# Optimization experiments

Measured on AMD Instinct MI355X. Metric: run time of the kernel, lower is better.

Reference implementation:

```python
import jax, jax.numpy as jnp
import numpy as np

V, D, B, S = 32000, 1024, 4, 2048
EPS = 1e-12  # matches torch F.normalize eps


def setup_inputs() -> dict:
    key = jax.random.key(0)
    k1, k2, k3 = jax.random.split(key, 3)
    init_embed = jax.random.normal(k1, (V, D), dtype=jnp.float32)
    scale = np.sqrt(D).astype(np.float32)  # default scale = sqrt(embed_dim)
    norm = jnp.maximum(jnp.linalg.norm(init_embed, axis=-1, keepdims=True), EPS)
    in_weight = scale * (init_embed / norm)            # [V, D]
    out_weight = init_embed.T                          # [D, V]
    inputs = jax.random.randint(k2, (B, S), 0, V)      # token ids
    embeds = jax.random.normal(k3, (B, S, D), dtype=jnp.float32)
    return {"inputs": inputs, "embeds": embeds, "in_weight": in_weight, "out_weight": out_weight}


def reference(inputs, embeds, in_weight, out_weight):
    # embed(): one_hot @ in_weight is mathematically an index gather
    embedded = jnp.take(in_weight, inputs, axis=0)          # [B, S, D]
    # unembed(): dense matmul against transposed embedding table
    logits = jnp.einsum('bsd,dv->bsv', embeds, out_weight)  # [B, S, V]
    return embedded, logits
```

## Files before the change

### kernel.cpp

```cpp
#include <hip/hip_runtime.h>
#include <hip/hip_bf16.h>
#include <stdint.h>

#define V_SZ 32000
#define D_SZ 1024
#define M_SZ 8192

typedef __attribute__((ext_vector_type(8))) short bf16x8;
typedef __attribute__((ext_vector_type(4))) float f32x4;
typedef __attribute__((ext_vector_type(16))) float f32x16;

static __device__ __forceinline__ unsigned short f32_to_bf16_rne(float f) {
    union { float f; uint32_t u; } v; v.f = f;
    uint32_t u = v.u;
    uint32_t lsb = (u >> 16) & 1;
    u += 0x7fffu + lsb;
    return (unsigned short)(u >> 16);
}

__global__ void gather_rows(const int* __restrict__ ids,
                            const float* __restrict__ table,
                            float* __restrict__ out) {
    int row = blockIdx.x;
    int id  = ids[row];
    const f32x4* src = (const f32x4*)(table + (size_t)id * D_SZ);
    f32x4*       dst = (f32x4*)(out + (size_t)row * D_SZ);
    __builtin_nontemporal_store(src[threadIdx.x], &dst[threadIdx.x]);
}

__global__ void cast_f32_bf16(const float* __restrict__ in,
                              unsigned short* __restrict__ out, int n8) {
    int i = blockIdx.x * blockDim.x + threadIdx.x;
    int stride = gridDim.x * blockDim.x;
    for (; i < n8; i += stride) {
        const float4* p = (const float4*)(in + (size_t)i * 8);
        float4 a = p[0], b = p[1];
        union { unsigned short s[8]; uint4 v; } r;
        r.s[0] = f32_to_bf16_rne(a.x); r.s[1] = f32_to_bf16_rne(a.y);
        r.s[2] = f32_to_bf16_rne(a.z); r.s[3] = f32_to_bf16_rne(a.w);
        r.s[4] = f32_to_bf16_rne(b.x); r.s[5] = f32_to_bf16_rne(b.y);
        r.s[6] = f32_to_bf16_rne(b.z); r.s[7] = f32_to_bf16_rne(b.w);
        ((uint4*)out)[i] = r.v;
    }
}

__global__ void transpose_cast(const float* __restrict__ w,
                               unsigned short* __restrict__ bt) {
    __shared__ unsigned short tile[32][34];
    int n0 = blockIdx.x * 32;
    int k0 = blockIdx.y * 32;
    int r = threadIdx.x >> 5;
    int c = threadIdx.x & 31;
#pragma unroll
    for (int rr = 0; rr < 32; rr += 8) {
        float v = w[(size_t)(k0 + r + rr) * V_SZ + (n0 + c)];
        tile[c][r + rr] = f32_to_bf16_rne(v);
    }
    __syncthreads();
    int nl = threadIdx.x >> 3;
    int ks = threadIdx.x & 7;
    union { unsigned short s[4]; uint2 v; } r2;
#pragma unroll
    for (int j = 0; j < 4; ++j) r2.s[j] = tile[nl][ks * 4 + j];
    ((uint2*)(bt + (size_t)(n0 + nl) * D_SZ + k0))[ks] = r2.v;
}

#define BM 256
#define BN 256
#define BK 64
#define NSTEP (D_SZ / BK)

static __device__ __forceinline__ void gload_lds16(const unsigned short* g, void* lds) {
    __builtin_amdgcn_global_load_lds(
        (const __attribute__((address_space(1))) void*)g,
        (__attribute__((address_space(3))) void*)lds,
        16, 0, 0);
}

__global__ __launch_bounds__(512, 2)
void gemm_persist(const unsigned short* __restrict__ A,
                  const unsigned short* __restrict__ Bt,
                  float* __restrict__ C) {
    __shared__ __align__(16) char lds[131072];

    const int tid  = threadIdx.x;
    const int lane = tid & 63;
    const int w    = tid >> 6;
    const int wr   = w >> 2;
    const int wc   = w & 3;

    const int bid = blockIdx.x;
    const int xcd = bid & 7;
    const int jb  = bid >> 3;
    const int bm0 = (xcd * 4 + (jb & 3)) * BM;
    const int q0  = jb >> 2;
    const int ntiles = (bid < 160) ? 16 : 15;

    const int hi0  = tid >> 7;
    const int row0 = tid & 127;
    const int dstO = hi0 * 2048 + row0 * 16;
    const unsigned short* gA = A  + (size_t)(bm0 + row0) * D_SZ + hi0 * 8;
    const unsigned short* gA1 = gA + (size_t)128 * D_SZ;
    const unsigned short* gBc = Bt + (size_t)(q0 * BN + row0) * D_SZ + hi0 * 8;
    const size_t bn_stride = (size_t)8 * BN * D_SZ;

#define STG(ptr, slotbase) do { \
    gload_lds16((ptr),      (char*)lds + (slotbase) + dstO); \
    gload_lds16((ptr) + 32, (char*)lds + (slotbase) + dstO + 8192); } while (0)

    STG(gBc,                           32768);
    STG(gBc + (size_t)128 * D_SZ,      32768 + 16384);
    STG(gA,                            0);
    STG(gA1,                           16384);
    STG(gBc + 64,                      65536 + 32768);
    STG(gBc + (size_t)128 * D_SZ + 64, 65536 + 32768 + 16384);
    STG(gA + 64,                       65536);
    asm volatile("s_waitcnt vmcnt(6)" ::: "memory");
    __builtin_amdgcn_s_barrier();

    f32x16 acc[4][2];
#pragma unroll
    for (int m = 0; m < 4; ++m)
#pragma unroll
        for (int n = 0; n < 2; ++n)
#pragma unroll
            for (int e = 0; e < 16; ++e) acc[m][n][e] = 0.0f;

    bf16x8 a[2][4];
    bf16x8 b[2][4];

    const int base_f = (lane >> 5) * 2048 + (lane & 31) * 16;

#define LDA(mi2, kk, QM) (*(const bf16x8*)(abuf + (kk) * 4096 + ((QM) * 2 + (mi2)) * 512 + base_f))
#define LDB(ni, kk)      (*(const bf16x8*)(bbuf + (kk) * 4096 + (ni) * 512 + base_f))

#define MFMA_Q(QM, QN) \
    __builtin_amdgcn_s_setprio(1); \
    _Pragma("unroll") for (int kk = 0; kk < 4; ++kk) \
    _Pragma("unroll") for (int mi2 = 0; mi2 < 2; ++mi2) \
        acc[(QM) * 2 + mi2][QN] = __builtin_amdgcn_mfma_f32_32x32x16_bf16( \
            a[mi2][kk], b[QN][kk], acc[(QM) * 2 + mi2][QN], 0, 0, 0); \
    __builtin_amdgcn_s_setprio(0);

#define MIDSYNC \
    __builtin_amdgcn_sched_barrier(0); \
    __builtin_amdgcn_s_barrier();

    const int crow = bm0 + wr * 128 + (lane >> 5) * 4;
    const int ccol_f = wc * 64 + (lane & 31);

    for (int r = 0; r < ntiles; ++r) {
        const unsigned short* gBn = gBc + bn_stride;
        const bool last = (r == ntiles - 1);

        for (int t = 0; t < NSTEP; ++t) {
            const int   dbuf = (t & 1) << 16;
            const char* abuf = (const char*)lds + dbuf + wr * 16384;
            const char* bbuf = (const char*)lds + dbuf + 32768
                               + (wc >> 1) * 16384 + (wc & 1) * 1024;
            const int nslot = (dbuf ^ 65536);

            a[0][0] = LDA(0, 0, 0); a[0][1] = LDA(0, 1, 0);
            a[0][2] = LDA(0, 2, 0); a[0][3] = LDA(0, 3, 0);
            a[1][0] = LDA(1, 0, 0); a[1][1] = LDA(1, 1, 0);
            a[1][2] = LDA(1, 2, 0); a[1][3] = LDA(1, 3, 0);
            b[0][0] = LDB(0, 0); b[0][1] = LDB(0, 1);
            b[0][2] = LDB(0, 2); b[0][3] = LDB(0, 3);
            if (!(last && t == 15)) STG(gA1 + ((t + 1) & 15) * 64, nslot + 16384);
            MIDSYNC;
            MFMA_Q(0, 0);
            __builtin_amdgcn_s_barrier();

            b[1][0] = LDB(1, 0); b[1][1] = LDB(1, 1);
            b[1][2] = LDB(1, 2); b[1][3] = LDB(1, 3);
            MIDSYNC;
            MFMA_Q(0, 1);
            __builtin_amdgcn_s_barrier();

            a[0][0] = LDA(0, 0, 1); a[0][1] = LDA(0, 1, 1);
            a[0][2] = LDA(0, 2, 1); a[0][3] = LDA(0, 3, 1);
            a[1][0] = LDA(1, 0, 1); a[1][1] = LDA(1, 1, 1);
            a[1][2] = LDA(1, 2, 1); a[1][3] = LDA(1, 3, 1);
            if (t < 14 || !last) {
                const unsigned short* pb = (t < 14) ? gBc + (t + 2) * 64
                                                    : gBn + (t - 14) * 64;
                STG(pb, dbuf + 32768);
            }
            MIDSYNC;
            MFMA_Q(1, 1);
            __builtin_amdgcn_s_barrier();

            if (t < 14 || !last) {
                const unsigned short* pb = (t < 14) ? gBc + (t + 2) * 64
                                                    : gBn + (t - 14) * 64;
                STG(pb + (size_t)128 * D_SZ, dbuf + 32768 + 16384);
                STG(gA + ((t + 2) & 15) * 64, dbuf);
            }
            MFMA_Q(1, 0);
            if (last && t >= 14) { asm volatile("s_waitcnt vmcnt(0)" ::: "memory"); }
            else                 { asm volatile("s_waitcnt vmcnt(6)" ::: "memory"); }
            __builtin_amdgcn_s_barrier();
        }

        const int ccol = (q0 + 8 * r) * BN + ccol_f;
#pragma unroll
        for (int mi = 0; mi < 4; ++mi)
#pragma unroll
            for (int ni = 0; ni < 2; ++ni) {
                float* base = C + (size_t)(crow + mi * 32) * V_SZ + (ccol + ni * 32);
#pragma unroll
                for (int e = 0; e < 16; ++e) {
                    int roff = (e & 3) + 8 * (e >> 2);
                    __builtin_nontemporal_store(acc[mi][ni][e], base + (size_t)roff * V_SZ);
                }
            }
#pragma unroll
        for (int m = 0; m < 4; ++m)
#pragma unroll
            for (int n = 0; n < 2; ++n)
#pragma unroll
                for (int e = 0; e < 16; ++e) acc[m][n][e] = 0.0f;

        gBc = gBn;
    }
#undef STG
#undef LDA
#undef LDB
#undef MFMA_Q
#undef MIDSYNC
}

extern "C" void kernel_launch(void* const* d_in, const int* in_sizes, int n_in,
                              void* d_out, int out_size, void* d_ws, size_t ws_size,
                              hipStream_t stream) {
    const int*   ids        = (const int*)d_in[0];
    const float* embeds     = (const float*)d_in[1];
    const float* in_weight  = (const float*)d_in[2];
    const float* out_weight = (const float*)d_in[3];

    float* out_embedded = (float*)d_out;
    float* out_logits   = (float*)d_out + (size_t)M_SZ * D_SZ;

    unsigned short* Abf  = (unsigned short*)d_ws;
    unsigned short* Btbf = Abf + (size_t)M_SZ * D_SZ;

    gather_rows<<<M_SZ, 256, 0, stream>>>(ids, in_weight, out_embedded);
    cast_f32_bf16<<<2048, 256, 0, stream>>>(embeds, Abf, M_SZ * D_SZ / 8);
    transpose_cast<<<dim3(V_SZ / 32, D_SZ / 32), 256, 0, stream>>>(out_weight, Btbf);
    gemm_persist<<<dim3(256), 512, 0, stream>>>(Abf, Btbf, out_logits);
}
```

Before: 676.7 us.

## Restructure GEMM inner loop to two half-phases with fewer barriers

Replaces the four barrier-separated MFMA quadrants per k-step with two phases, each loading A and B fragments and then issuing two quadrant MFMA groups under raised priority. A-tile prefetch now loads both halves one step ahead into the alternate buffer, and the B halves are issued together. The vmcnt threshold and prologue change to match. The aim is to cut s_barrier and sched_barrier overhead per step. The cost is less interleaving of LDS reads with MFMAs and a changed prefetch distance for A, which could expose more memory latency or cause LDS hazards.

```diff
diff --git a/kernel.cpp b/kernel.cpp
--- a/kernel.cpp
+++ b/kernel.cpp
@@ -99,7 +99,7 @@
     const int hi0  = tid >> 7;
     const int row0 = tid & 127;
     const int dstO = hi0 * 2048 + row0 * 16;
-    const unsigned short* gA = A  + (size_t)(bm0 + row0) * D_SZ + hi0 * 8;
+    const unsigned short* gA  = A  + (size_t)(bm0 + row0) * D_SZ + hi0 * 8;
     const unsigned short* gA1 = gA + (size_t)128 * D_SZ;
     const unsigned short* gBc = Bt + (size_t)(q0 * BN + row0) * D_SZ + hi0 * 8;
     const size_t bn_stride = (size_t)8 * BN * D_SZ;
@@ -108,14 +108,13 @@
     gload_lds16((ptr),      (char*)lds + (slotbase) + dstO); \
     gload_lds16((ptr) + 32, (char*)lds + (slotbase) + dstO + 8192); } while (0)
 
-    STG(gBc,                           32768);
-    STG(gBc + (size_t)128 * D_SZ,      32768 + 16384);
-    STG(gA,                            0);
-    STG(gA1,                           16384);
-    STG(gBc + 64,                      65536 + 32768);
-    STG(gBc + (size_t)128 * D_SZ + 64, 65536 + 32768 + 16384);
-    STG(gA + 64,                       65536);
-    asm volatile("s_waitcnt vmcnt(6)" ::: "memory");
+    STG(gA,                                 0);
+    STG(gA1,                                16384);
+    STG(gBc,                                32768);
+    STG(gBc + (size_t)128 * D_SZ,           49152);
+    STG(gBc + 64,                           65536 + 32768);
+    STG(gBc + (size_t)128 * D_SZ + 64,      65536 + 49152);
+    asm volatile("s_waitcnt vmcnt(0)" ::: "memory");
     __builtin_amdgcn_s_barrier();
 
     f32x16 acc[4][2];
@@ -135,16 +134,10 @@
 #define LDB(ni, kk)      (*(const bf16x8*)(bbuf + (kk) * 4096 + (ni) * 512 + base_f))
 
 #define MFMA_Q(QM, QN) \
-    __builtin_amdgcn_s_setprio(1); \
     _Pragma("unroll") for (int kk = 0; kk < 4; ++kk) \
     _Pragma("unroll") for (int mi2 = 0; mi2 < 2; ++mi2) \
         acc[(QM) * 2 + mi2][QN] = __builtin_amdgcn_mfma_f32_32x32x16_bf16( \
-            a[mi2][kk], b[QN][kk], acc[(QM) * 2 + mi2][QN], 0, 0, 0); \
-    __builtin_amdgcn_s_setprio(0);
-
-#define MIDSYNC \
-    __builtin_amdgcn_sched_barrier(0); \
-    __builtin_amdgcn_s_barrier();
+            a[mi2][kk], b[QN][kk], acc[(QM) * 2 + mi2][QN], 0, 0, 0);
 
     const int crow = bm0 + wr * 128 + (lane >> 5) * 4;
     const int ccol_f = wc * 64 + (lane & 31);
@@ -154,11 +147,11 @@
         const bool last = (r == ntiles - 1);
 
         for (int t = 0; t < NSTEP; ++t) {
-            const int   dbuf = (t & 1) << 16;
-            const char* abuf = (const char*)lds + dbuf + wr * 16384;
-            const char* bbuf = (const char*)lds + dbuf + 32768
-                               + (wc >> 1) * 16384 + (wc & 1) * 1024;
-            const int nslot = (dbuf ^ 65536);
+            const int   dbuf  = (t & 1) << 16;
+            const int   nslot = dbuf ^ 65536;
+            const char* abuf  = (const char*)lds + dbuf + wr * 16384;
+            const char* bbuf  = (const char*)lds + dbuf + 32768
+                                + (wc >> 1) * 16384 + (wc & 1) * 1024;
 
             a[0][0] = LDA(0, 0, 0); a[0][1] = LDA(0, 1, 0);
             a[0][2] = LDA(0, 2, 0); a[0][3] = LDA(0, 3, 0);
@@ -166,15 +159,16 @@
             a[1][2] = LDA(1, 2, 0); a[1][3] = LDA(1, 3, 0);
             b[0][0] = LDB(0, 0); b[0][1] = LDB(0, 1);
             b[0][2] = LDB(0, 2); b[0][3] = LDB(0, 3);
-            if (!(last && t == 15)) STG(gA1 + ((t + 1) & 15) * 64, nslot + 16384);
-            MIDSYNC;
-            MFMA_Q(0, 0);
-            __builtin_amdgcn_s_barrier();
-
             b[1][0] = LDB(1, 0); b[1][1] = LDB(1, 1);
             b[1][2] = LDB(1, 2); b[1][3] = LDB(1, 3);
-            MIDSYNC;
+            if (!(last && t == 15)) {
+                STG(gA  + ((t + 1) & 15) * 64, nslot);
+                STG(gA1 + ((t + 1) & 15) * 64, nslot + 16384);
+            }
+            __builtin_amdgcn_s_setprio(1);
+            MFMA_Q(0, 0);
             MFMA_Q(0, 1);
+            __builtin_amdgcn_s_setprio(0);
             __builtin_amdgcn_s_barrier();
 
             a[0][0] = LDA(0, 0, 1); a[0][1] = LDA(0, 1, 1);
@@ -185,20 +179,14 @@
                 const unsigned short* pb = (t < 14) ? gBc + (t + 2) * 64
                                                     : gBn + (t - 14) * 64;
                 STG(pb, dbuf + 32768);
+                STG(pb + (size_t)128 * D_SZ, dbuf + 49152);
             }
-            MIDSYNC;
+            __builtin_amdgcn_s_setprio(1);
             MFMA_Q(1, 1);
-            __builtin_amdgcn_s_barrier();
-
-            if (t < 14 || !last) {
-                const unsigned short* pb = (t < 14) ? gBc + (t + 2) * 64
-                                                    : gBn + (t - 14) * 64;
-                STG(pb + (size_t)128 * D_SZ, dbuf + 32768 + 16384);
-                STG(gA + ((t + 2) & 15) * 64, dbuf);
-            }
             MFMA_Q(1, 0);
+            __builtin_amdgcn_s_setprio(0);
             if (last && t >= 14) { asm volatile("s_waitcnt vmcnt(0)" ::: "memory"); }
-            else                 { asm volatile("s_waitcnt vmcnt(6)" ::: "memory"); }
+            else                 { asm volatile("s_waitcnt vmcnt(4)" ::: "memory"); }
             __builtin_amdgcn_s_barrier();
         }
 
@@ -227,7 +215,6 @@
 #undef LDA
 #undef LDB
 #undef MFMA_Q
-#undef MIDSYNC
 }
 
 extern "C" void kernel_launch(void* const* d_in, const int* in_sizes, int n_in,
```

Result: slower. 708.0 us (+4.6%).
